# Optimization experiments

Hardware: AMD Instinct MI355X
Metric: run time of the kernel (lower is better)

The kernel has to match this reference:

```python
import jax, jax.numpy as jnp
import numpy as np

N_NODES = 100000
N_EDGES = 1600000
NUM_GRAPHS = 4096
EPS = 1e-5


def _glorot(key, shape):
    fan_in, fan_out = shape[0], shape[1]
    lim = float(np.sqrt(6.0 / (fan_in + fan_out)))
    return jax.random.uniform(key, shape, jnp.float32, -lim, lim)


def setup_inputs() -> dict:
    key = jax.random.key(0)
    ks = jax.random.split(key, 32)
    inp = {}
    inp['x'] = jax.random.normal(ks[0], (N_NODES, 32), jnp.float32)
    inp['edge_attr'] = jax.random.uniform(ks[1], (N_EDGES, 8), jnp.float32)
    inp['edge_index'] = jax.random.randint(ks[2], (2, N_EDGES), 0, N_NODES, jnp.int32)
    inp['batch'] = jnp.sort(jax.random.randint(ks[3], (N_NODES,), 0, NUM_GRAPHS, jnp.int32))
    inp['num_graphs'] = NUM_GRAPHS
    # node/edge embeddings
    inp['Wn'] = _glorot(ks[4], (32, 64)); inp['bn_'] = jnp.zeros((64,), jnp.float32)
    inp['We'] = _glorot(ks[5], (8, 16)); inp['be_'] = jnp.zeros((16,), jnp.float32)
    # conv1: 2*64+16=144 -> 128 -> 64
    inp['W1a'] = _glorot(ks[6], (144, 128)); inp['b1a'] = jnp.zeros((128,), jnp.float32)
    inp['W1b'] = _glorot(ks[7], (128, 64)); inp['b1b'] = jnp.zeros((64,), jnp.float32)
    # conv2: 2*64+16=144 -> 64 -> 32
    inp['W2a'] = _glorot(ks[8], (144, 64)); inp['b2a'] = jnp.zeros((64,), jnp.float32)
    inp['W2b'] = _glorot(ks[9], (64, 32)); inp['b2b'] = jnp.zeros((32,), jnp.float32)
    # conv3: 2*32+16=80 -> 32 -> 16
    inp['W3a'] = _glorot(ks[10], (80, 32)); inp['b3a'] = jnp.zeros((32,), jnp.float32)
    inp['W3b'] = _glorot(ks[11], (32, 16)); inp['b3b'] = jnp.zeros((16,), jnp.float32)
    # batchnorm affine params
    inp['g1'] = jnp.ones((64,), jnp.float32); inp['beta1'] = jnp.zeros((64,), jnp.float32)
    inp['g2'] = jnp.ones((32,), jnp.float32); inp['beta2'] = jnp.zeros((32,), jnp.float32)
    inp['g3'] = jnp.ones((16,), jnp.float32); inp['beta3'] = jnp.zeros((16,), jnp.float32)
    # final fc 16 -> 12
    inp['Wfc'] = _glorot(ks[12], (16, 12)); inp['bfc'] = jnp.zeros((12,), jnp.float32)
    return inp


def _conv(x, e_emb, src, dst, Wa, ba, Wb, bb, n_nodes):
    # PyG: x_i = x[target]=x[dst], x_j = x[source]=x[src]; message MLP; mean-aggregate at dst
    m = jnp.concatenate([x[dst], x[src], e_emb], axis=1)      # [E, 2*in+edge]
    m = jax.nn.relu(m @ Wa + ba) @ Wb + bb                    # [E, out]
    s = jax.ops.segment_sum(m, dst, num_segments=n_nodes)
    cnt = jax.ops.segment_sum(jnp.ones((m.shape[0], 1), m.dtype), dst, num_segments=n_nodes)
    return s / jnp.maximum(cnt, 1.0)


def _batchnorm(x, g, b):
    mu = jnp.mean(x, axis=0)
    var = jnp.mean(jnp.square(x - mu), axis=0)
    return (x - mu) * jax.lax.rsqrt(var + EPS) * g + b


def reference(x, edge_attr, edge_index, batch, num_graphs,
              Wn, bn_, We, be_, W1a, b1a, W1b, b1b, W2a, b2a, W2b, b2b,
              W3a, b3a, W3b, b3b, g1, beta1, g2, beta2, g3, beta3, Wfc, bfc):
    n_nodes = x.shape[0]
    src, dst = edge_index[0], edge_index[1]
    e_emb = jax.nn.relu(edge_attr @ We + be_)                 # [E, 16]
    h = jax.nn.relu(x @ Wn + bn_)                             # [N, 64]
    h = _conv(h, e_emb, src, dst, W1a, b1a, W1b, b1b, n_nodes)
    h = jax.nn.relu(_batchnorm(h, g1, beta1))
    h = _conv(h, e_emb, src, dst, W2a, b2a, W2b, b2b, n_nodes)
    h = jax.nn.relu(_batchnorm(h, g2, beta2))
    h = _conv(h, e_emb, src, dst, W3a, b3a, W3b, b3b, n_nodes)
    h = jax.nn.relu(_batchnorm(h, g3, beta3))
    # global mean pool per graph
    s = jax.ops.segment_sum(h, batch, num_segments=num_graphs)
    cnt = jax.ops.segment_sum(jnp.ones((n_nodes, 1), h.dtype), batch, num_segments=num_graphs)
    pooled = s / jnp.maximum(cnt, 1.0)                        # [G, 16]
    return jax.nn.sigmoid(pooled @ Wfc + bfc)                 # [G, 12]
```

## Files before the change

### kernel.cpp

```cpp
#include <hip/hip_runtime.h>
#include <hip/hip_bf16.h>
#include <cstdio>


#define N_NODES 100000
#define N_EDGES 1600000
#define NUM_GRAPHS 4096

typedef unsigned short u16;
typedef unsigned int u32;
typedef _Float16 h2 __attribute__((ext_vector_type(2)));

#if defined(__has_builtin)
#if __has_builtin(__builtin_amdgcn_fdot2)
#define DOT2(a, b, c) __builtin_amdgcn_fdot2((a), (b), (c), false)
#endif
#endif
#ifndef DOT2
#define DOT2(a, b, c) ((c) + (float)(a).x * (float)(b).x + (float)(a).y * (float)(b).y)
#endif

__device__ __forceinline__ float b2f(u16 u) { union { u32 i; float f; } c; c.i = ((u32)u) << 16; return c.f; }
__device__ __forceinline__ float b2f_lo(u32 u) { union { u32 i; float f; } c; c.i = u << 16; return c.f; }
__device__ __forceinline__ float b2f_hi(u32 u) { union { u32 i; float f; } c; c.i = u & 0xffff0000u; return c.f; }
__device__ __forceinline__ u16 f2b(float f) {
    __hip_bfloat16 h = __float2bfloat16(f);
    return *reinterpret_cast<u16*>(&h);
}

template <int CPL>
__device__ __forceinline__ void ld_bf16(const u16* base, float out[CPL]) {
    if constexpr (CPL == 1) {
        out[0] = b2f(*base);
    } else {
        u32 v = *(const u32*)base;
        out[0] = b2f_lo(v); out[1] = b2f_hi(v);
    }
}
template <int CPL>
__device__ __forceinline__ void ld_f32(const float* base, float out[CPL]) {
    if constexpr (CPL == 1) {
        out[0] = *base;
    } else {
        float2 v = *(const float2*)base;
        out[0] = v.x; out[1] = v.y;
    }
}

__global__ __launch_bounds__(256) void hist_k(const int* __restrict__ dst, int* __restrict__ hist) {
    int e = blockIdx.x * 256 + threadIdx.x;
    if (e < N_EDGES) atomicAdd(&hist[dst[e]], 1);
}

__global__ __launch_bounds__(256) void scan_part_k(const int* __restrict__ hist,
        int* __restrict__ excl, int* __restrict__ bsum) {
    __shared__ int sm[256];
    int t = threadIdx.x, b = blockIdx.x;
    int base = b * 1024 + t * 4;
    int v0 = (base + 0 < N_NODES) ? hist[base + 0] : 0;
    int v1 = (base + 1 < N_NODES) ? hist[base + 1] : 0;
    int v2 = (base + 2 < N_NODES) ? hist[base + 2] : 0;
    int v3 = (base + 3 < N_NODES) ? hist[base + 3] : 0;
    int tsum = v0 + v1 + v2 + v3;
    sm[t] = tsum;
    __syncthreads();
    for (int o = 1; o < 256; o <<= 1) {
        int x = (t >= o) ? sm[t - o] : 0;
        __syncthreads();
        sm[t] += x;
        __syncthreads();
    }
    int texcl = sm[t] - tsum;
    if (base + 0 < N_NODES) excl[base + 0] = texcl;
    if (base + 1 < N_NODES) excl[base + 1] = texcl + v0;
    if (base + 2 < N_NODES) excl[base + 2] = texcl + v0 + v1;
    if (base + 3 < N_NODES) excl[base + 3] = texcl + v0 + v1 + v2;
    if (t == 255) bsum[b] = sm[255];
}

__global__ __launch_bounds__(256) void scan_top_k(int* __restrict__ bsum, int* __restrict__ boff,
        int nb, int* __restrict__ row_ptr_last) {
    __shared__ int sm[256];
    int t = threadIdx.x;
    int v = (t < nb) ? bsum[t] : 0;
    sm[t] = v;
    __syncthreads();
    for (int o = 1; o < 256; o <<= 1) {
        int x = (t >= o) ? sm[t - o] : 0;
        __syncthreads();
        sm[t] += x;
        __syncthreads();
    }
    if (t < nb) boff[t] = sm[t] - v;
    if (t == 0) *row_ptr_last = sm[255];
}

__global__ __launch_bounds__(256) void scan_add_k(int* __restrict__ excl, const int* __restrict__ boff,
        int* __restrict__ row_ptr, int* __restrict__ cursor) {
    int i = blockIdx.x * 256 + threadIdx.x;
    if (i >= N_NODES) return;
    int s = excl[i] + boff[i >> 10];
    row_ptr[i] = s;
    cursor[i] = s;
}

__global__ __launch_bounds__(256) void scatter2_k(const int* __restrict__ src, const int* __restrict__ dst,
        const float* __restrict__ ea, const float* __restrict__ We, const float* __restrict__ be,
        int* __restrict__ cursor, int* __restrict__ srcs, _Float16* __restrict__ e16s) {
    int idx = blockIdx.x * 256 + threadIdx.x;
    int e = idx >> 4, k = idx & 15;
    int lane = threadIdx.x & 63;
    int p = 0;
    if (k == 0) {
        p = atomicAdd(&cursor[dst[e]], 1);
        srcs[p] = src[e];
    }
    p = __shfl(p, lane & 48);
    float4 a0 = *(const float4*)(ea + (size_t)e * 8);
    float4 a1 = *(const float4*)(ea + (size_t)e * 8 + 4);
    float acc = be[k];
    acc += a0.x * We[0 * 16 + k];
    acc += a0.y * We[1 * 16 + k];
    acc += a0.z * We[2 * 16 + k];
    acc += a0.w * We[3 * 16 + k];
    acc += a1.x * We[4 * 16 + k];
    acc += a1.y * We[5 * 16 + k];
    acc += a1.z * We[6 * 16 + k];
    acc += a1.w * We[7 * 16 + k];
    e16s[(size_t)p * 16 + k] = (_Float16)fmaxf(acc, 0.f);
}

__global__ __launch_bounds__(256) void ubound_k(const int* __restrict__ row_ptr, int* __restrict__ sn) {
    int u = blockIdx.x * 256 + threadIdx.x;
    if (u > 25000) return;
    if (u == 25000) { sn[u] = N_NODES; return; }
    int target = u * 64;
    int lo = 0, hi = N_NODES;
    while (lo < hi) {
        int mid = (lo + hi) >> 1;
        if (row_ptr[mid] >= target) hi = mid; else lo = mid + 1;
    }
    sn[u] = lo;
}

__global__ __launch_bounds__(256) void node_emb2_k(const float* __restrict__ x,
        const float* __restrict__ Wn, const float* __restrict__ bn_, float* __restrict__ h) {
    constexpr int C = 64, F = 32, TILE = 64;
    __shared__ float xs[TILE * F];
    const int t = threadIdx.x;
    const int grp = t / C;
    const int c = t % C;
    float w[F];
#pragma unroll
    for (int k = 0; k < F; ++k) w[k] = Wn[(size_t)k * 64 + c];
    const float bias = bn_[c];
    const float4* xsrc = (const float4*)x;
    float4* xs4 = (float4*)xs;

    for (int v0 = blockIdx.x * TILE; v0 < N_NODES; v0 += gridDim.x * TILE) {
        __syncthreads();
        for (int i = t; i < TILE * F / 4; i += 256) {
            int vv = v0 + (i * 4) / F;
            float4 val;
            if (vv < N_NODES) val = xsrc[(size_t)v0 * (F / 4) + i];
            else { val.x = val.y = val.z = val.w = 0.f; }
            xs4[i] = val;
        }
        __syncthreads();
        const int base = grp * 16;
        const int nmax = (N_NODES - v0 - base >= 16) ? 16
                        : (N_NODES - v0 - base > 0 ? N_NODES - v0 - base : 0);
        for (int n = 0; n < nmax; ++n) {
            const int v = v0 + base + n;
            const float4* xr4 = (const float4*)&xs[(base + n) * F];
            float a0 = bias, a1 = 0.f, a2 = 0.f, a3 = 0.f;
#pragma unroll
            for (int k4 = 0; k4 < F / 4; ++k4) {
                float4 hv = xr4[k4];
                a0 += hv.x * w[4 * k4 + 0];
                a1 += hv.y * w[4 * k4 + 1];
                a2 += hv.z * w[4 * k4 + 2];
                a3 += hv.w * w[4 * k4 + 3];
            }
            h[(size_t)v * 64 + c] = fmaxf((a0 + a1) + (a2 + a3), 0.f);
        }
    }
}

template <int F, int H, bool BN>
__global__ __launch_bounds__(256) void proj_k(const float* __restrict__ h,
        const float* __restrict__ Wa, const float* __restrict__ ba,
        const float* __restrict__ stats, const float* __restrict__ g, const float* __restrict__ beta,
        float* __restrict__ Pd, u16* __restrict__ Ps) {
    constexpr int C2 = 2 * H;
    constexpr int NPB = 256 / C2;
    constexpr int TILE = 16 * NPB;
    __shared__ float hs[TILE][F];
    __shared__ float sc[BN ? F : 1];
    __shared__ float shv[BN ? F : 1];
    const int t = threadIdx.x;
    if constexpr (BN) {
        if (t < F) {
            const float invN = 1.0f / (float)N_NODES;
            float mu = stats[t] * invN;
            float ex2 = stats[F + t] * invN;
            float var = fmaxf(ex2 - mu * mu, 0.f);
            float rs = rsqrtf(var + 1e-5f);
            float scale = rs * g[t];
            sc[t] = scale;
            shv[t] = beta[t] - mu * scale;
        }
    }
    const int grp = t / C2;
    const int c = t % C2;
    const bool is_src = (c >= H);
    const int cc = is_src ? (c - H) : c;
    float w[F];
    const float* wcol = Wa + (size_t)(is_src ? F : 0) * H + cc;
#pragma unroll
    for (int k = 0; k < F; ++k) w[k] = wcol[(size_t)k * H];
    const float bias = is_src ? 0.f : ba[cc];

    for (int v0 = blockIdx.x * TILE; v0 < N_NODES; v0 += gridDim.x * TILE) {
        __syncthreads();
        for (int i = t; i < TILE * F; i += 256) {
            int vv = v0 + i / F;
            float val = (vv < N_NODES) ? h[(size_t)vv * F + (i % F)] : 0.f;
            if constexpr (BN) val = fmaxf(val * sc[i % F] + shv[i % F], 0.f);
            hs[i / F][i % F] = val;
        }
        __syncthreads();
        const int base = grp * 16;
        const int nmax = (N_NODES - v0 - base >= 16) ? 16
                        : (N_NODES - v0 - base > 0 ? N_NODES - v0 - base : 0);
#pragma unroll 2
        for (int n = 0; n < nmax; ++n) {
            const int v = v0 + base + n;
            const float4* hr4 = (const float4*)hs[base + n];
            float a0 = bias, a1 = 0.f, a2 = 0.f, a3 = 0.f;
#pragma unroll
            for (int k4 = 0; k4 < F / 4; ++k4) {
                float4 hv = hr4[k4];
                a0 += hv.x * w[4 * k4 + 0];
                a1 += hv.y * w[4 * k4 + 1];
                a2 += hv.z * w[4 * k4 + 2];
                a3 += hv.w * w[4 * k4 + 3];
            }
            float acc = (a0 + a1) + (a2 + a3);
            if (is_src) Ps[(size_t)v * H + cc] = f2b(acc);
            else        Pd[(size_t)v * H + cc] = acc;
        }
    }
}

template <int H>
__global__ __launch_bounds__(256) void conv_k(
        const int* __restrict__ sn, const int* __restrict__ row_ptr,
        const int* __restrict__ srcs, const _Float16* __restrict__ e16s,
        float* __restrict__ Pd, const u16* __restrict__ Ps,
        const float* __restrict__ Wae) {
    constexpr int SL = (H >= 64) ? 64 : 32;
    constexpr int NPW = 64 / SL;
    constexpr int CPL = H / SL;
    const int wave = threadIdx.x >> 6, lane = threadIdx.x & 63;
    const int sub = lane / SL;
    const int sl = lane % SL;
    const int c0 = sl * CPL;
    h2 w2h[8][CPL];
#pragma unroll
    for (int k2 = 0; k2 < 8; ++k2)
#pragma unroll
        for (int j = 0; j < CPL; ++j) {
            h2 t;
            t.x = (_Float16)Wae[(2 * k2) * H + c0 + j];
            t.y = (_Float16)Wae[(2 * k2 + 1) * H + c0 + j];
            w2h[k2][j] = t;
        }

    const int uid = (blockIdx.x * 4 + wave) * NPW + sub;
    const int vbeg = sn[uid], vend = sn[uid + 1];

    for (int v = vbeg; v < vend; ++v) {
        const int vv = (SL == 64) ? __builtin_amdgcn_readfirstlane(v) : v;
        float pd[CPL], acc[CPL];
        ld_f32<CPL>(&Pd[(size_t)vv * H + c0], pd);
#pragma unroll
        for (int j = 0; j < CPL; ++j) acc[j] = 0.f;
        const int p0 = row_ptr[vv], p1 = row_ptr[vv + 1];
        const int deg = p1 - p0;

        auto edge = [&](uint4 ra, uint4 rb, const float ps[CPL]) {
            union { u32 u; h2 h; } cv;
            h2 ev[8];
            cv.u = ra.x; ev[0] = cv.h; cv.u = ra.y; ev[1] = cv.h;
            cv.u = ra.z; ev[2] = cv.h; cv.u = ra.w; ev[3] = cv.h;
            cv.u = rb.x; ev[4] = cv.h; cv.u = rb.y; ev[5] = cv.h;
            cv.u = rb.z; ev[6] = cv.h; cv.u = rb.w; ev[7] = cv.h;
            float z[CPL];
#pragma unroll
            for (int j = 0; j < CPL; ++j) z[j] = pd[j] + ps[j];
#pragma unroll
            for (int k2 = 0; k2 < 8; ++k2)
#pragma unroll
                for (int j = 0; j < CPL; ++j) z[j] = DOT2(ev[k2], w2h[k2][j], z[j]);
#pragma unroll
            for (int j = 0; j < CPL; ++j) acc[j] += fmaxf(z[j], 0.f);
        };

        int p = p0;
        for (; p + 3 < p1; p += 4) {
            int s0 = srcs[p], s1 = srcs[p + 1], s2 = srcs[p + 2], s3 = srcs[p + 3];
            const uint4* e0 = (const uint4*)(e16s + (size_t)p * 16);
            uint4 a0 = e0[0], a1 = e0[1];
            uint4 b0 = e0[2], b1 = e0[3];
            uint4 g0 = e0[4], g1 = e0[5];
            uint4 d0 = e0[6], d1 = e0[7];
            float ps0[CPL], ps1[CPL], ps2[CPL], ps3[CPL];
            ld_bf16<CPL>(&Ps[(size_t)s0 * H + c0], ps0);
            ld_bf16<CPL>(&Ps[(size_t)s1 * H + c0], ps1);
            ld_bf16<CPL>(&Ps[(size_t)s2 * H + c0], ps2);
            ld_bf16<CPL>(&Ps[(size_t)s3 * H + c0], ps3);
            edge(a0, a1, ps0);
            edge(b0, b1, ps1);
            edge(g0, g1, ps2);
            edge(d0, d1, ps3);
        }
        for (; p < p1; ++p) {
            int s0 = srcs[p];
            const uint4* e0 = (const uint4*)(e16s + (size_t)p * 16);
            uint4 a0 = e0[0], a1 = e0[1];
            float ps0[CPL];
            ld_bf16<CPL>(&Ps[(size_t)s0 * H + c0], ps0);
            edge(a0, a1, ps0);
        }

        const float invd = (deg > 0) ? 1.f / (float)deg : 0.f;
        if constexpr (CPL == 2) {
            float2 o; o.x = acc[0] * invd; o.y = acc[1] * invd;
            *(float2*)&Pd[(size_t)vv * H + c0] = o;
        } else {
            Pd[(size_t)vv * H + c0] = acc[0] * invd;
        }
    }
}

template <int H, int Fo>
__global__ __launch_bounds__(256) void matvec2_k(const float* __restrict__ m,
        const int* __restrict__ row_ptr,
        const float* __restrict__ Wb, const float* __restrict__ bb,
        float* __restrict__ y, float* __restrict__ stats) {
    constexpr int FoC = (Fo < 32) ? Fo : 32;
    constexpr int CG = Fo / FoC;
    constexpr int NPW = 32 / FoC;
    constexpr int NG = 4 / CG;
    constexpr int SLOTS = NG * NPW;
    constexpr int KH = H / 2;
    constexpr int TILE = 4096 / H;
    constexpr int J = TILE / SLOTS;

    __shared__ float hs[TILE * H];
    __shared__ int ptile[TILE + 1];
    __shared__ float sh[2 * Fo];

    const int t = threadIdx.x;
    const int wave = t >> 6, lane = t & 63;
    const int kh = lane >> 5;
    const int r = lane & 31;
    const int c_lo = r % FoC;
    const int s = r / FoC;
    const int cg = wave % CG;
    const int ng = wave / CG;
    const int c = cg * FoC + c_lo;
    const int slot = ng * NPW + s;

    for (int i = t; i < 2 * Fo; i += 256) sh[i] = 0.f;

    float w[KH];
#pragma unroll
    for (int k = 0; k < KH; ++k) w[k] = Wb[(size_t)(kh * KH + k) * Fo + c];
    const float bias = bb[c];
    float s1 = 0.f, s2 = 0.f;

    const float4* msrc = (const float4*)m;
    float4* hs4 = (float4*)hs;

    for (int v0 = blockIdx.x * TILE; v0 < N_NODES; v0 += gridDim.x * TILE) {
        __syncthreads();
#pragma unroll
        for (int q = t; q < 1024; q += 256) {
            int node = (q * 4) / H;
            float4 val;
            if (v0 + node < N_NODES) val = msrc[(size_t)v0 * (H / 4) + q];
            else { val.x = val.y = val.z = val.w = 0.f; }
            hs4[q] = val;
        }
        for (int i = t; i <= TILE; i += 256) {
            int v = v0 + i;
            ptile[i] = row_ptr[v < N_NODES ? v : N_NODES];
        }
        __syncthreads();

        for (int j = 0; j < J; ++j) {
            const int n = slot + j * SLOTS;
            const int v = v0 + n;
            const float4* hr4 = (const float4*)&hs[n * H + kh * KH];
            float a0 = 0.f, a1 = 0.f, a2 = 0.f, a3 = 0.f;
#pragma unroll
            for (int k4 = 0; k4 < KH / 4; ++k4) {
                float4 hv = hr4[k4];
                a0 += hv.x * w[4 * k4 + 0];
                a1 += hv.y * w[4 * k4 + 1];
                a2 += hv.z * w[4 * k4 + 2];
                a3 += hv.w * w[4 * k4 + 3];
            }
            float half = (a0 + a1) + (a2 + a3);
            float total = half + __shfl_xor(half, 32) + bias;
            if (kh == 0 && v < N_NODES) {
                const int deg = ptile[n + 1] - ptile[n];
                float val = (deg > 0) ? total : 0.f;
                y[(size_t)v * Fo + c] = val;
                s1 += val; s2 += val * val;
            }
        }
    }

    __syncthreads();
    if (kh == 0) {
        atomicAdd(&sh[c], s1);
        atomicAdd(&sh[Fo + c], s2);
    }
    __syncthreads();
    if (t < 2 * Fo) atomicAdd(&stats[t], sh[t]);
}

__global__ __launch_bounds__(256) void pool_bn_k(const float* __restrict__ y,
        const float* __restrict__ stats, const float* __restrict__ g, const float* __restrict__ beta,
        const int* __restrict__ batch, float* __restrict__ pool, int* __restrict__ gcnt) {
    int idx = blockIdx.x * 256 + threadIdx.x;
    if (idx >= N_NODES * 16) return;
    int v = idx >> 4, c = idx & 15;
    const float invN = 1.0f / (float)N_NODES;
    float mu = stats[c] * invN;
    float ex2 = stats[16 + c] * invN;
    float var = fmaxf(ex2 - mu * mu, 0.f);
    float rs = rsqrtf(var + 1e-5f);
    float val = fmaxf((y[idx] - mu) * rs * g[c] + beta[c], 0.f);
    int b = batch[v];
    atomicAdd(&pool[b * 16 + c], val);
    if (c == 0) atomicAdd(&gcnt[b], 1);
}

__global__ __launch_bounds__(256) void out_k(const float* __restrict__ pool,
        const int* __restrict__ gcnt, const float* __restrict__ Wfc,
        const float* __restrict__ bfc, float* __restrict__ out) {
    int idx = blockIdx.x * 256 + threadIdx.x;
    if (idx >= NUM_GRAPHS * 12) return;
    int g = idx / 12, o = idx % 12;
    int cnt = gcnt[g];
    float inv = 1.0f / (float)(cnt > 0 ? cnt : 1);
    float acc = bfc[o];
#pragma unroll
    for (int k = 0; k < 16; ++k) acc += pool[g * 16 + k] * inv * Wfc[k * 12 + o];
    out[idx] = 1.0f / (1.0f + expf(-acc));
}

extern "C" void kernel_launch(void* const* d_in, const int* in_sizes, int n_in,
                              void* d_out, int out_size, void* d_ws, size_t ws_size,
                              hipStream_t stream) {
    const size_t N = N_NODES, E = N_EDGES, G = NUM_GRAPHS;
    const float* x = (const float*)d_in[0];
    const float* ea = (const float*)d_in[1];
    const int* ei = (const int*)d_in[2];
    const int* srcv = ei;
    const int* dstv = ei + E;
    const int* batch = (const int*)d_in[3];
    const float* Wn = (const float*)d_in[5];  const float* bn_ = (const float*)d_in[6];
    const float* We = (const float*)d_in[7];  const float* be_ = (const float*)d_in[8];
    const float* W1a = (const float*)d_in[9]; const float* b1a = (const float*)d_in[10];
    const float* W1b = (const float*)d_in[11]; const float* b1b = (const float*)d_in[12];
    const float* W2a = (const float*)d_in[13]; const float* b2a = (const float*)d_in[14];
    const float* W2b = (const float*)d_in[15]; const float* b2b = (const float*)d_in[16];
    const float* W3a = (const float*)d_in[17]; const float* b3a = (const float*)d_in[18];
    const float* W3b = (const float*)d_in[19]; const float* b3b = (const float*)d_in[20];
    const float* g1 = (const float*)d_in[21]; const float* be1 = (const float*)d_in[22];
    const float* g2 = (const float*)d_in[23]; const float* be2 = (const float*)d_in[24];
    const float* g3 = (const float*)d_in[25]; const float* be3 = (const float*)d_in[26];
    const float* Wfc = (const float*)d_in[27]; const float* bfc = (const float*)d_in[28];

    char* base = (char*)d_ws;
    size_t off = 0;
    auto take = [&](size_t bytes) { size_t o = off; off += (bytes + 255) & ~(size_t)255; return o; };
    int* hist = (int*)(base + take(N * 4));
    int* cursor = (int*)(base + take(N * 4));
    int* row_ptr = (int*)(base + take((N + 1) * 4));
    int* bsum = (int*)(base + take(256 * 4));
    int* boff = (int*)(base + take(256 * 4));
    int* sn = (int*)(base + take(25001 * 4));
    int* srcs = (int*)(base + take(E * 4));
    float* hbuf = (float*)(base + take(N * 64 * 4));
    float* Pd = (float*)(base + take(N * 128 * 4));
    u16* Ps = (u16*)(base + take(N * 128 * 2));
    _Float16* e16s = (_Float16*)(base + take(E * 16 * 2));
    float* stats = (float*)(base + take(256 * 4));
    float* pool = (float*)(base + take(G * 16 * 4));
    int* gcnt = (int*)(base + take(G * 4));
    if (off > ws_size) {
        fprintf(stderr, "kernel_launch: ws too small: need %zu have %zu\n", off, ws_size);
        return;
    }

    const int NB = (N_NODES + 1023) / 1024;

    hipMemsetAsync(hist, 0, N * 4, stream);
    hist_k<<<dim3((E + 255) / 256), dim3(256), 0, stream>>>(dstv, hist);
    scan_part_k<<<dim3(NB), dim3(256), 0, stream>>>(hist, cursor, bsum);
    scan_top_k<<<dim3(1), dim3(256), 0, stream>>>(bsum, boff, NB, &row_ptr[N_NODES]);
    scan_add_k<<<dim3((N + 255) / 256), dim3(256), 0, stream>>>(cursor, boff, row_ptr, cursor);
    scatter2_k<<<dim3(E * 16 / 256), dim3(256), 0, stream>>>(srcv, dstv, ea, We, be_, cursor, srcs, e16s);
    ubound_k<<<dim3((25001 + 255) / 256), dim3(256), 0, stream>>>(row_ptr, sn);

    node_emb2_k<<<dim3(1563), dim3(256), 0, stream>>>(x, Wn, bn_, hbuf);

    proj_k<64, 128, false><<<dim3(6250), dim3(256), 0, stream>>>(hbuf, W1a, b1a, nullptr, nullptr, nullptr, Pd, Ps);
    conv_k<128><<<dim3(6250), dim3(256), 0, stream>>>(sn, row_ptr, srcs, e16s, Pd, Ps, W1a + 128 * 128);
    hipMemsetAsync(stats, 0, 256 * 4, stream);
    matvec2_k<128, 64><<<dim3(1024), dim3(256), 0, stream>>>(Pd, row_ptr, W1b, b1b, hbuf, stats);

    proj_k<64, 64, true><<<dim3(3125), dim3(256), 0, stream>>>(hbuf, W2a, b2a, stats, g1, be1, Pd, Ps);
    conv_k<64><<<dim3(6250), dim3(256), 0, stream>>>(sn, row_ptr, srcs, e16s, Pd, Ps, W2a + 128 * 64);
    hipMemsetAsync(stats, 0, 256 * 4, stream);
    matvec2_k<64, 32><<<dim3(1024), dim3(256), 0, stream>>>(Pd, row_ptr, W2b, b2b, hbuf, stats);

    proj_k<32, 32, true><<<dim3(1563), dim3(256), 0, stream>>>(hbuf, W3a, b3a, stats, g2, be2, Pd, Ps);
    conv_k<32><<<dim3(3125), dim3(256), 0, stream>>>(sn, row_ptr, srcs, e16s, Pd, Ps, W3a + 64 * 32);
    hipMemsetAsync(stats, 0, 256 * 4, stream);
    matvec2_k<32, 16><<<dim3(1024), dim3(256), 0, stream>>>(Pd, row_ptr, W3b, b3b, hbuf, stats);

    hipMemsetAsync(pool, 0, G * 16 * 4, stream);
    hipMemsetAsync(gcnt, 0, G * 4, stream);
    pool_bn_k<<<dim3((N * 16 + 255) / 256), dim3(256), 0, stream>>>(hbuf, stats, g3, be3, batch, pool, gcnt);
    out_k<<<dim3((G * 12 + 255) / 256), dim3(256), 0, stream>>>(pool, gcnt, Wfc, bfc, (float*)d_out);
}
```

Measured before the change: 1.003 ms.

## Store edge embeddings in original order and gather via sorted edge ids

Splits the combined scatter/embedding kernel in two. One kernel does the atomic CSR scatter and records sorted edge ids and sources. A separate kernel writes edge embeddings in original edge order with coalesced stores. The conv kernels now read embeddings indirectly through the sorted edge-id array, which removes the scattered embedding writes. The cost is random 32-byte gathers in each of the three conv passes plus an extra index read.

New measurement: 1.007 ms. No clear change (+0.4%).

```diff
diff --git a/kernel.cpp b/kernel.cpp
--- a/kernel.cpp
+++ b/kernel.cpp
@@ -104,18 +104,34 @@
     cursor[i] = s;
 }
 
-__global__ __launch_bounds__(256) void scatter2_k(const int* __restrict__ src, const int* __restrict__ dst,
-        const float* __restrict__ ea, const float* __restrict__ We, const float* __restrict__ be,
-        int* __restrict__ cursor, int* __restrict__ srcs, _Float16* __restrict__ e16s) {
+__global__ __launch_bounds__(256) void scatter_k(const int* __restrict__ src, const int* __restrict__ dst,
+        int* __restrict__ cursor, int* __restrict__ sorted_eid, int* __restrict__ srcs) {
+    int e = blockIdx.x * 256 + threadIdx.x;
+    if (e < N_EDGES) {
+        int p = atomicAdd(&cursor[dst[e]], 1);
+        sorted_eid[p] = e;
+        srcs[p] = src[e];
+    }
+}
+
+__global__ __launch_bounds__(256) void ubound_k(const int* __restrict__ row_ptr, int* __restrict__ sn) {
+    int u = blockIdx.x * 256 + threadIdx.x;
+    if (u > 25000) return;
+    if (u == 25000) { sn[u] = N_NODES; return; }
+    int target = u * 64;
+    int lo = 0, hi = N_NODES;
+    while (lo < hi) {
+        int mid = (lo + hi) >> 1;
+        if (row_ptr[mid] >= target) hi = mid; else lo = mid + 1;
+    }
+    sn[u] = lo;
+}
+
+__global__ __launch_bounds__(256) void edge_emb_o_k(const float* __restrict__ ea,
+        const float* __restrict__ We, const float* __restrict__ be,
+        _Float16* __restrict__ e16o) {
     int idx = blockIdx.x * 256 + threadIdx.x;
     int e = idx >> 4, k = idx & 15;
-    int lane = threadIdx.x & 63;
-    int p = 0;
-    if (k == 0) {
-        p = atomicAdd(&cursor[dst[e]], 1);
-        srcs[p] = src[e];
-    }
-    p = __shfl(p, lane & 48);
     float4 a0 = *(const float4*)(ea + (size_t)e * 8);
     float4 a1 = *(const float4*)(ea + (size_t)e * 8 + 4);
     float acc = be[k];
@@ -127,20 +143,7 @@
     acc += a1.y * We[5 * 16 + k];
     acc += a1.z * We[6 * 16 + k];
     acc += a1.w * We[7 * 16 + k];
-    e16s[(size_t)p * 16 + k] = (_Float16)fmaxf(acc, 0.f);
-}
-
-__global__ __launch_bounds__(256) void ubound_k(const int* __restrict__ row_ptr, int* __restrict__ sn) {
-    int u = blockIdx.x * 256 + threadIdx.x;
-    if (u > 25000) return;
-    if (u == 25000) { sn[u] = N_NODES; return; }
-    int target = u * 64;
-    int lo = 0, hi = N_NODES;
-    while (lo < hi) {
-        int mid = (lo + hi) >> 1;
-        if (row_ptr[mid] >= target) hi = mid; else lo = mid + 1;
-    }
-    sn[u] = lo;
+    e16o[(size_t)idx] = (_Float16)fmaxf(acc, 0.f);
 }
 
 __global__ __launch_bounds__(256) void node_emb2_k(const float* __restrict__ x,
@@ -256,7 +259,8 @@
 template <int H>
 __global__ __launch_bounds__(256) void conv_k(
         const int* __restrict__ sn, const int* __restrict__ row_ptr,
-        const int* __restrict__ srcs, const _Float16* __restrict__ e16s,
+        const int* __restrict__ srcs, const int* __restrict__ eid,
+        const _Float16* __restrict__ e16o,
         float* __restrict__ Pd, const u16* __restrict__ Ps,
         const float* __restrict__ Wae) {
     constexpr int SL = (H >= 64) ? 64 : 32;
@@ -310,11 +314,15 @@
         int p = p0;
         for (; p + 3 < p1; p += 4) {
             int s0 = srcs[p], s1 = srcs[p + 1], s2 = srcs[p + 2], s3 = srcs[p + 3];
-            const uint4* e0 = (const uint4*)(e16s + (size_t)p * 16);
-            uint4 a0 = e0[0], a1 = e0[1];
-            uint4 b0 = e0[2], b1 = e0[3];
-            uint4 g0 = e0[4], g1 = e0[5];
-            uint4 d0 = e0[6], d1 = e0[7];
+            int e0i = eid[p], e1i = eid[p + 1], e2i = eid[p + 2], e3i = eid[p + 3];
+            const uint4* q0 = (const uint4*)(e16o + (size_t)e0i * 16);
+            const uint4* q1 = (const uint4*)(e16o + (size_t)e1i * 16);
+            const uint4* q2 = (const uint4*)(e16o + (size_t)e2i * 16);
+            const uint4* q3 = (const uint4*)(e16o + (size_t)e3i * 16);
+            uint4 a0 = q0[0], a1 = q0[1];
+            uint4 b0 = q1[0], b1 = q1[1];
+            uint4 g0 = q2[0], g1 = q2[1];
+            uint4 d0 = q3[0], d1 = q3[1];
             float ps0[CPL], ps1[CPL], ps2[CPL], ps3[CPL];
             ld_bf16<CPL>(&Ps[(size_t)s0 * H + c0], ps0);
             ld_bf16<CPL>(&Ps[(size_t)s1 * H + c0], ps1);
@@ -327,8 +335,9 @@
         }
         for (; p < p1; ++p) {
             int s0 = srcs[p];
-            const uint4* e0 = (const uint4*)(e16s + (size_t)p * 16);
-            uint4 a0 = e0[0], a1 = e0[1];
+            int e0i = eid[p];
+            const uint4* q0 = (const uint4*)(e16o + (size_t)e0i * 16);
+            uint4 a0 = q0[0], a1 = q0[1];
             float ps0[CPL];
             ld_bf16<CPL>(&Ps[(size_t)s0 * H + c0], ps0);
             edge(a0, a1, ps0);
@@ -496,11 +505,12 @@
     int* bsum = (int*)(base + take(256 * 4));
     int* boff = (int*)(base + take(256 * 4));
     int* sn = (int*)(base + take(25001 * 4));
+    int* sorted = (int*)(base + take(E * 4));
     int* srcs = (int*)(base + take(E * 4));
     float* hbuf = (float*)(base + take(N * 64 * 4));
     float* Pd = (float*)(base + take(N * 128 * 4));
     u16* Ps = (u16*)(base + take(N * 128 * 2));
-    _Float16* e16s = (_Float16*)(base + take(E * 16 * 2));
+    _Float16* e16o = (_Float16*)(base + take(E * 16 * 2));
     float* stats = (float*)(base + take(256 * 4));
     float* pool = (float*)(base + take(G * 16 * 4));
     int* gcnt = (int*)(base + take(G * 4));
@@ -516,23 +526,24 @@
     scan_part_k<<<dim3(NB), dim3(256), 0, stream>>>(hist, cursor, bsum);
     scan_top_k<<<dim3(1), dim3(256), 0, stream>>>(bsum, boff, NB, &row_ptr[N_NODES]);
     scan_add_k<<<dim3((N + 255) / 256), dim3(256), 0, stream>>>(cursor, boff, row_ptr, cursor);
-    scatter2_k<<<dim3(E * 16 / 256), dim3(256), 0, stream>>>(srcv, dstv, ea, We, be_, cursor, srcs, e16s);
+    scatter_k<<<dim3((E + 255) / 256), dim3(256), 0, stream>>>(srcv, dstv, cursor, sorted, srcs);
     ubound_k<<<dim3((25001 + 255) / 256), dim3(256), 0, stream>>>(row_ptr, sn);
 
+    edge_emb_o_k<<<dim3(E * 16 / 256), dim3(256), 0, stream>>>(ea, We, be_, e16o);
     node_emb2_k<<<dim3(1563), dim3(256), 0, stream>>>(x, Wn, bn_, hbuf);
 
     proj_k<64, 128, false><<<dim3(6250), dim3(256), 0, stream>>>(hbuf, W1a, b1a, nullptr, nullptr, nullptr, Pd, Ps);
-    conv_k<128><<<dim3(6250), dim3(256), 0, stream>>>(sn, row_ptr, srcs, e16s, Pd, Ps, W1a + 128 * 128);
+    conv_k<128><<<dim3(6250), dim3(256), 0, stream>>>(sn, row_ptr, srcs, sorted, e16o, Pd, Ps, W1a + 128 * 128);
     hipMemsetAsync(stats, 0, 256 * 4, stream);
     matvec2_k<128, 64><<<dim3(1024), dim3(256), 0, stream>>>(Pd, row_ptr, W1b, b1b, hbuf, stats);
 
     proj_k<64, 64, true><<<dim3(3125), dim3(256), 0, stream>>>(hbuf, W2a, b2a, stats, g1, be1, Pd, Ps);
-    conv_k<64><<<dim3(6250), dim3(256), 0, stream>>>(sn, row_ptr, srcs, e16s, Pd, Ps, W2a + 128 * 64);
+    conv_k<64><<<dim3(6250), dim3(256), 0, stream>>>(sn, row_ptr, srcs, sorted, e16o, Pd, Ps, W2a + 128 * 64);
     hipMemsetAsync(stats, 0, 256 * 4, stream);
     matvec2_k<64, 32><<<dim3(1024), dim3(256), 0, stream>>>(Pd, row_ptr, W2b, b2b, hbuf, stats);
 
     proj_k<32, 32, true><<<dim3(1563), dim3(256), 0, stream>>>(hbuf, W3a, b3a, stats, g2, be2, Pd, Ps);
-    conv_k<32><<<dim3(3125), dim3(256), 0, stream>>>(sn, row_ptr, srcs, e16s, Pd, Ps, W3a + 64 * 32);
+    conv_k<32><<<dim3(3125), dim3(256), 0, stream>>>(sn, row_ptr, srcs, sorted, e16o, Pd, Ps, W3a + 64 * 32);
     hipMemsetAsync(stats, 0, 256 * 4, stream);
     matvec2_k<32, 16><<<dim3(1024), dim3(256), 0, stream>>>(Pd, row_ptr, W3b, b3b, hbuf, stats);
 
```
